# Kernel optimization log

Hardware: AMD Instinct MI355X
Metric: run time of the kernel (lower is better)

## Reference

```python
import jax, jax.numpy as jnp
import numpy as np

N, S, F, E, H, O, L, FE = 8, 1024, 64, 512, 8, 64, 6, 4
HD = E // H
FF = FE * E


def setup_inputs() -> dict:
    key = jax.random.key(0)
    ks = iter(jax.random.split(key, 40))
    def rn(shape, s=0.02):
        return jax.random.normal(next(ks), shape, jnp.float32) * s
    return {
        'x': jax.random.normal(next(ks), (N, F, S), jnp.float32),
        'W_first': rn((F, E)), 'b_first': jnp.zeros((E,), jnp.float32),
        'pos_emb': rn((S, E)),
        'Wq': rn((L, HD, HD)), 'bq': jnp.zeros((L, HD), jnp.float32),
        'Wk': rn((L, HD, HD)), 'bk': jnp.zeros((L, HD), jnp.float32),
        'Wv': rn((L, HD, HD)), 'bv': jnp.zeros((L, HD), jnp.float32),
        'Wo': rn((L, E, E)), 'bo': jnp.zeros((L, E), jnp.float32),
        'g1': jnp.ones((L, E), jnp.float32), 'be1': jnp.zeros((L, E), jnp.float32),
        'Wf1': rn((L, E, FF)), 'bf1': jnp.zeros((L, FF), jnp.float32),
        'Wf2': rn((L, FF, E)), 'bf2': jnp.zeros((L, E), jnp.float32),
        'g2': jnp.ones((L, E), jnp.float32), 'be2': jnp.zeros((L, E), jnp.float32),
        'Wfin': rn((E, O)), 'bfin': jnp.zeros((O,), jnp.float32),
    }


def layernorm(x, g, b, eps=1e-5):
    m = jnp.mean(x, axis=-1, keepdims=True)
    v = jnp.mean(jnp.square(x - m), axis=-1, keepdims=True)
    return (x - m) * jax.lax.rsqrt(v + eps) * g + b


def reference(x, W_first, b_first, pos_emb, Wq, bq, Wk, bk, Wv, bv, Wo, bo,
              g1, be1, Wf1, bf1, Wf2, bf2, g2, be2, Wfin, bfin):
    # x: (N, F, S) -> (N, S, F)
    h = jax.nn.relu(jnp.einsum('nfs,fe->nse', x, W_first) + b_first) + pos_emb[None]
    scale = E ** 0.5  # note: module scales by sqrt(embed_size), not sqrt(head_dim)
    for i in range(L):
        t = h.reshape(N, S, H, HD)
        q = jnp.einsum('nshd,de->nshe', t, Wq[i]) + bq[i]
        k = jnp.einsum('nshd,de->nshe', t, Wk[i]) + bk[i]
        v = jnp.einsum('nshd,de->nshe', t, Wv[i]) + bv[i]
        energy = jnp.einsum('nqhd,nkhd->nhqk', q, k)  # (N,H,S,S)
        att = jax.nn.softmax(energy / scale, axis=-1)
        o = jnp.einsum('nhqk,nkhd->nqhd', att, v).reshape(N, S, E)
        o = jnp.einsum('nse,ef->nsf', o, Wo[i]) + bo[i]
        hx = layernorm(o + h, g1[i], be1[i])
        ff = jax.nn.relu(jnp.einsum('nse,ef->nsf', hx, Wf1[i]) + bf1[i])
        ff = jnp.einsum('nsf,fe->nse', ff, Wf2[i]) + bf2[i]
        h = layernorm(ff + hx, g2[i], be2[i])
    # Conv1d kernel_size=1 == pointwise linear over channels; output (N, O, S)
    return jnp.einsum('nse,eo->nos', h, Wfin) + bfin[None, :, None]
```

## Files before the change

### kernel.cpp

```cpp
#include <hip/hip_runtime.h>
#include <hip/hip_bf16.h>
#include <math.h>

#define N_ 8
#define S_ 1024
#define F_ 64
#define E_ 512
#define H_ 8
#define O_ 64
#define L_ 6
#define HD_ 64
#define FF_ 2048
#define SCALE_ 0.044194173824159216f
#define LOG2E_ 1.4426950408889634f
#define QSCALE_ (SCALE_ * LOG2E_)

typedef unsigned short u16;
typedef __attribute__((ext_vector_type(8))) unsigned short u16x8;
typedef __attribute__((ext_vector_type(8))) short short8;
typedef __attribute__((ext_vector_type(4))) float floatx4;

__device__ __forceinline__ u16 f2b(float f) {
    union { float f; unsigned u; } v; v.f = f;
    unsigned u = v.u;
    unsigned r = (u + 0x7FFFu + ((u >> 16) & 1u)) >> 16;
    return (u16)r;
}
__device__ __forceinline__ u16 f2b_fast(float f) {
    union { float f; unsigned u; } v; v.f = f;
    return (u16)((v.u + 0x8000u) >> 16);
}
__device__ __forceinline__ int pperm(int row) {
    return ((2 * (row >> 2) + 5 * (row & 3)) & 7) | ((row & 2) << 2);
}

__global__ __launch_bounds__(256) void first_mfma(
    const float* __restrict__ x, const u16* __restrict__ wt,
    const float* __restrict__ bf, const float* __restrict__ pe,
    float* __restrict__ hout, u16* __restrict__ hb)
{
    __shared__ u16 a_s[128][72];
    int t = threadIdx.x;
    int w = t >> 6, lane = t & 63, quad = lane >> 4, c16 = lane & 15;
    int rowhalf = w >> 1, colhalf = w & 1;
    int col0 = blockIdx.x * 128;
    int row0 = blockIdx.y * 128;
    int n = row0 >> 10, s0 = row0 & 1023;

    const float* xb = x + (size_t)n * F_ * S_ + s0;
    #pragma unroll
    for (int i = 0; i < 8; i++) {
        int pos = (t + i * 256) * 4;
        int f = pos >> 7, sl = pos & 127;
        float4 v = *(const float4*)&xb[(size_t)f * S_ + sl];
        a_s[sl + 0][f] = f2b_fast(v.x);
        a_s[sl + 1][f] = f2b_fast(v.y);
        a_s[sl + 2][f] = f2b_fast(v.z);
        a_s[sl + 3][f] = f2b_fast(v.w);
    }
    __syncthreads();

    floatx4 acc[4][4];
    #pragma unroll
    for (int mt = 0; mt < 4; mt++)
        #pragma unroll
        for (int nt = 0; nt < 4; nt++) acc[mt][nt] = (floatx4){0.f, 0.f, 0.f, 0.f};

    #pragma unroll
    for (int ks = 0; ks < 2; ks++) {
        short8 af[4], bfr[4];
        #pragma unroll
        for (int mt = 0; mt < 4; mt++)
            af[mt] = *(const short8*)&a_s[rowhalf * 64 + mt * 16 + c16][ks * 32 + quad * 8];
        #pragma unroll
        for (int nt = 0; nt < 4; nt++)
            bfr[nt] = *(const short8*)&wt[(size_t)(col0 + colhalf * 64 + nt * 16 + c16) * F_
                                          + ks * 32 + quad * 8];
        #pragma unroll
        for (int mt = 0; mt < 4; mt++)
            #pragma unroll
            for (int nt = 0; nt < 4; nt++)
                acc[mt][nt] = __builtin_amdgcn_mfma_f32_16x16x32_bf16(
                    af[mt], bfr[nt], acc[mt][nt], 0, 0, 0);
    }

    #pragma unroll
    for (int nt = 0; nt < 4; nt++) {
        int col = col0 + colhalf * 64 + nt * 16 + c16;
        float bv = bf[col];
        #pragma unroll
        for (int mt = 0; mt < 4; mt++) {
            #pragma unroll
            for (int r = 0; r < 4; r++) {
                size_t row = (size_t)row0 + rowhalf * 64 + mt * 16 + quad * 4 + r;
                int s = (int)(row & 1023);
                float v = fmaxf(acc[mt][nt][r] + bv, 0.f) + pe[(size_t)s * E_ + col];
                hout[row * E_ + col] = v;
                hb[row * E_ + col] = f2b_fast(v);
            }
        }
    }
}

__global__ __launch_bounds__(256) void wcast_t(
    const float* __restrict__ W0, u16* __restrict__ Wt0, int K, int Nc)
{
    __shared__ float tile[32][33];
    int t = threadIdx.x;
    int bx = blockIdx.x, by = blockIdx.y;
    const float* W = W0 + (size_t)blockIdx.z * K * Nc;
    u16* Wt = Wt0 + (size_t)blockIdx.z * K * Nc;
    #pragma unroll
    for (int i = 0; i < 4; i++) {
        int q = t + i * 256; int r = q >> 5, c = q & 31;
        tile[r][c] = W[(size_t)(by * 32 + r) * Nc + bx * 32 + c];
    }
    __syncthreads();
    #pragma unroll
    for (int i = 0; i < 4; i++) {
        int q = t + i * 256; int r = q >> 5, c = q & 31;
        Wt[(size_t)(bx * 32 + r) * K + by * 32 + c] = f2b(tile[c][r]);
    }
}

__global__ __launch_bounds__(256) void qkvw_cast(
    const float* __restrict__ Wq, const float* __restrict__ Wk,
    const float* __restrict__ Wv,
    u16* __restrict__ wqt, u16* __restrict__ wkt, u16* __restrict__ wvt)
{
    int l = blockIdx.x;
    int t = threadIdx.x;
    size_t off = (size_t)l * HD_ * HD_;
    #pragma unroll
    for (int i = 0; i < 16; i++) {
        int idx = t + i * 256;
        int e = idx >> 6, d = idx & 63;
        wqt[off + idx] = f2b(Wq[off + d * HD_ + e]);
        wkt[off + idx] = f2b(Wk[off + d * HD_ + e]);
        wvt[off + idx] = f2b(Wv[off + d * HD_ + e]);
    }
}

__global__ __launch_bounds__(256) void qkv_mfma(
    const u16* __restrict__ hb,
    const u16* __restrict__ wqt, const u16* __restrict__ wkt,
    const u16* __restrict__ wvt,
    const float* __restrict__ bq, const float* __restrict__ bk,
    const float* __restrict__ bv,
    u16* __restrict__ qo, u16* __restrict__ ko, u16* __restrict__ vo)
{
    __shared__ u16 a_s[256][72];
    int t = threadIdx.x;
    int w = t >> 6, lane = t & 63, quad = lane >> 4, c16 = lane & 15;
    size_t row0 = (size_t)blockIdx.x * 256;

    #pragma unroll
    for (int i = 0; i < 8; i++) {
        int q = t + i * 256; int r = q >> 3, c = q & 7;
        *(u16x8*)&a_s[r][c * 8] = *(const u16x8*)&hb[(row0 + r) * HD_ + c * 8];
    }
    __syncthreads();

    short8 af[4][2];
    #pragma unroll
    for (int mt = 0; mt < 4; mt++)
        #pragma unroll
        for (int ks = 0; ks < 2; ks++)
            af[mt][ks] = *(const short8*)&a_s[w * 64 + mt * 16 + c16][ks * 32 + quad * 8];

    const u16* wts[3] = {wqt, wkt, wvt};
    const float* bs[3] = {bq, bk, bv};
    u16* outs[3] = {qo, ko, vo};

    #pragma unroll
    for (int m = 0; m < 3; m++) {
        short8 bfr[4][2];
        #pragma unroll
        for (int nt = 0; nt < 4; nt++)
            #pragma unroll
            for (int ks = 0; ks < 2; ks++)
                bfr[nt][ks] = *(const short8*)&wts[m][(nt * 16 + c16) * HD_ + ks * 32 + quad * 8];
        floatx4 acc[4][4];
        #pragma unroll
        for (int mt = 0; mt < 4; mt++)
            #pragma unroll
            for (int nt = 0; nt < 4; nt++) acc[mt][nt] = (floatx4){0.f, 0.f, 0.f, 0.f};
        #pragma unroll
        for (int ks = 0; ks < 2; ks++)
            #pragma unroll
            for (int mt = 0; mt < 4; mt++)
                #pragma unroll
                for (int nt = 0; nt < 4; nt++)
                    acc[mt][nt] = __builtin_amdgcn_mfma_f32_16x16x32_bf16(
                        af[mt][ks], bfr[nt][ks], acc[mt][nt], 0, 0, 0);
        float osc = (m == 0) ? QSCALE_ : 1.0f;
        #pragma unroll
        for (int nt = 0; nt < 4; nt++) {
            float bv_ = bs[m][nt * 16 + c16];
            #pragma unroll
            for (int mt = 0; mt < 4; mt++)
                #pragma unroll
                for (int r = 0; r < 4; r++)
                    outs[m][(row0 + w * 64 + mt * 16 + quad * 4 + r) * HD_ + nt * 16 + c16] =
                        f2b_fast((acc[mt][nt][r] + bv_) * osc);
        }
    }
}

__global__ __launch_bounds__(256) void vtrans(
    const u16* __restrict__ vb, u16* __restrict__ vt)
{
    int bid = blockIdx.x;
    int st = bid & 15, hh = (bid >> 4) & 7, n = bid >> 7;
    __shared__ u16 tile[64][72];
    int t = threadIdx.x;
    #pragma unroll
    for (int i = 0; i < 2; i++) {
        int q = t + i * 256; int sl = q >> 3, c = q & 7;
        *(u16x8*)&tile[sl][c * 8] =
            *(const u16x8*)&vb[(((size_t)(n * S_ + st * 64 + sl)) * H_ + hh) * 64 + c * 8];
    }
    __syncthreads();
    #pragma unroll
    for (int i = 0; i < 2; i++) {
        int q = t + i * 256; int d = q >> 3, sc = q & 7;
        u16x8 v;
        #pragma unroll
        for (int j = 0; j < 8; j++) v[j] = tile[sc * 8 + j][d];
        *(u16x8*)&vt[((size_t)(n * H_ + hh) * 64 + d) * (size_t)S_ + st * 64 + sc * 8] = v;
    }
}

__global__ __launch_bounds__(256, 2) void attn_mfma(
    const u16* __restrict__ Q, const u16* __restrict__ K,
    const u16* __restrict__ Vt, u16* __restrict__ O)
{
    int bid = blockIdx.x;
    int qt = bid & 7, hh = (bid >> 3) & 7, n = bid >> 6;
    int t = threadIdx.x;
    int w = t >> 6, lane = t & 63, quad = lane >> 4, c16 = lane & 15;

    __shared__ u16 qp_s[128][72];
    __shared__ u16 k_s[64][72];
    __shared__ u16 vt_s[64][72];
    u16 (*p_s)[72] = &qp_s[w * 32];

    const size_t qkbase = (size_t)n * S_ * E_ + hh * 64;
    const size_t vtbase = ((size_t)(n * H_ + hh) * 64) * (size_t)S_;

    #pragma unroll
    for (int i = 0; i < 4; i++) {
        int q = t + i * 256; int r = q >> 3, c = q & 7;
        *(u16x8*)&qp_s[r][c * 8] =
            *(const u16x8*)&Q[qkbase + (size_t)(qt * 128 + r) * E_ + c * 8];
    }
    __syncthreads();

    short8 af[2][2];
    #pragma unroll
    for (int mt = 0; mt < 2; mt++)
        #pragma unroll
        for (int ks = 0; ks < 2; ks++)
            af[mt][ks] = *(const short8*)&qp_s[w * 32 + mt * 16 + c16][ks * 32 + quad * 8];

    const short8 ones = {(short)0x3F80, (short)0x3F80, (short)0x3F80, (short)0x3F80,
                         (short)0x3F80, (short)0x3F80, (short)0x3F80, (short)0x3F80};
    const int pr = pperm(c16);
    int pw[4];
    #pragma unroll
    for (int r = 0; r < 4; r++) pw[r] = pperm(quad * 4 + r);

    floatx4 oacc[2][4], lacc[2];
    #pragma unroll
    for (int mt = 0; mt < 2; mt++) {
        lacc[mt] = (floatx4){0.f, 0.f, 0.f, 0.f};
        #pragma unroll
        for (int nt = 0; nt < 4; nt++) oacc[mt][nt] = (floatx4){0.f, 0.f, 0.f, 0.f};
    }

    int ar = t >> 3, acq = (t & 7) * 8;
    u16x8 pk[2], pv[2];
    #pragma unroll
    for (int i = 0; i < 2; i++) {
        pk[i] = *(const u16x8*)&K[qkbase + (size_t)(ar + i * 32) * E_ + acq];
        pv[i] = *(const u16x8*)&Vt[vtbase + (size_t)(ar + i * 32) * S_ + acq];
    }

    for (int k0 = 0; k0 < S_; k0 += 64) {
        #pragma unroll
        for (int i = 0; i < 2; i++) {
            *(u16x8*)&k_s[ar + i * 32][acq] = pk[i];
            *(u16x8*)&vt_s[ar + i * 32][acq] = pv[i];
        }
        __syncthreads();
        if (k0 + 64 < S_) {
            #pragma unroll
            for (int i = 0; i < 2; i++) {
                pk[i] = *(const u16x8*)&K[qkbase + (size_t)(k0 + 64 + ar + i * 32) * E_ + acq];
                pv[i] = *(const u16x8*)&Vt[vtbase + (size_t)(ar + i * 32) * S_ + k0 + 64 + acq];
            }
        }

        floatx4 sc[2][4];
        #pragma unroll
        for (int mt = 0; mt < 2; mt++)
            #pragma unroll
            for (int nt = 0; nt < 4; nt++) sc[mt][nt] = (floatx4){0.f, 0.f, 0.f, 0.f};
        #pragma unroll
        for (int ks = 0; ks < 2; ks++) {
            short8 bfr[4];
            #pragma unroll
            for (int nt = 0; nt < 4; nt++)
                bfr[nt] = *(const short8*)&k_s[nt * 16 + c16][ks * 32 + quad * 8];
            #pragma unroll
            for (int mt = 0; mt < 2; mt++)
                #pragma unroll
                for (int nt = 0; nt < 4; nt++)
                    sc[mt][nt] = __builtin_amdgcn_mfma_f32_16x16x32_bf16(
                        af[mt][ks], bfr[nt], sc[mt][nt], 0, 0, 0);
        }

        #pragma unroll
        for (int mt = 0; mt < 2; mt++)
            #pragma unroll
            for (int nt = 0; nt < 4; nt++)
                #pragma unroll
                for (int r = 0; r < 4; r++)
                    p_s[mt * 16 + pw[r]][nt * 16 + c16] =
                        f2b_fast(exp2f(sc[mt][nt][r]));

        #pragma unroll
        for (int ks = 0; ks < 2; ks++) {
            short8 vf[4];
            #pragma unroll
            for (int nt = 0; nt < 4; nt++)
                vf[nt] = *(const short8*)&vt_s[nt * 16 + c16][ks * 32 + quad * 8];
            #pragma unroll
            for (int mt = 0; mt < 2; mt++) {
                short8 pf = *(const short8*)&p_s[mt * 16 + pr][ks * 32 + quad * 8];
                lacc[mt] = __builtin_amdgcn_mfma_f32_16x16x32_bf16(pf, ones, lacc[mt], 0, 0, 0);
                #pragma unroll
                for (int nt = 0; nt < 4; nt++)
                    oacc[mt][nt] = __builtin_amdgcn_mfma_f32_16x16x32_bf16(
                        pf, vf[nt], oacc[mt][nt], 0, 0, 0);
            }
        }
        __syncthreads();
    }

    #pragma unroll
    for (int mt = 0; mt < 2; mt++)
        #pragma unroll
        for (int r = 0; r < 4; r++) {
            float rl = 1.f / lacc[mt][r];
            int s = qt * 128 + w * 32 + mt * 16 + quad * 4 + r;
            size_t base = (size_t)(n * S_ + s) * E_ + hh * 64;
            #pragma unroll
            for (int nt = 0; nt < 4; nt++)
                O[base + nt * 16 + c16] = f2b_fast(oacc[mt][nt][r] * rl);
        }
}

template <int MT, bool RELU, bool HASRES, bool OUTF32, bool OUTBF16>
__global__ __launch_bounds__(256, 2) void gemm_mfma(
    const u16* __restrict__ A, const u16* __restrict__ Bt,
    const float* __restrict__ bias, const float* __restrict__ resid,
    float* __restrict__ outf, u16* __restrict__ outb, int M, int Nc, int K)
{
    constexpr int MTILES = MT / 32;
    __shared__ u16 a_s[MT][72];
    __shared__ u16 b_s[128][72];
    int t = threadIdx.x;
    int w = t >> 6, lane = t & 63, quad = lane >> 4, c16 = lane & 15;
    int rowhalf = w >> 1, colhalf = w & 1;
    size_t row0 = (size_t)blockIdx.y * MT;
    size_t col0 = (size_t)blockIdx.x * 128;

    floatx4 acc[MTILES][4];
    #pragma unroll
    for (int mt = 0; mt < MTILES; mt++)
        #pragma unroll
        for (int nt = 0; nt < 4; nt++) acc[mt][nt] = (floatx4){0.f, 0.f, 0.f, 0.f};

    int ar = t >> 3, acq = (t & 7) * 8;
    u16x8 pa[MTILES], pb[4];
    #pragma unroll
    for (int i = 0; i < MTILES; i++)
        pa[i] = *(const u16x8*)&A[(row0 + ar + i * 32) * K + acq];
    #pragma unroll
    for (int i = 0; i < 4; i++)
        pb[i] = *(const u16x8*)&Bt[(col0 + ar + i * 32) * K + acq];

    for (int k0 = 0; k0 < K; k0 += 64) {
        #pragma unroll
        for (int i = 0; i < MTILES; i++)
            *(u16x8*)&a_s[ar + i * 32][acq] = pa[i];
        #pragma unroll
        for (int i = 0; i < 4; i++)
            *(u16x8*)&b_s[ar + i * 32][acq] = pb[i];
        __syncthreads();
        if (k0 + 64 < K) {
            #pragma unroll
            for (int i = 0; i < MTILES; i++)
                pa[i] = *(const u16x8*)&A[(row0 + ar + i * 32) * K + k0 + 64 + acq];
            #pragma unroll
            for (int i = 0; i < 4; i++)
                pb[i] = *(const u16x8*)&Bt[(col0 + ar + i * 32) * K + k0 + 64 + acq];
        }
        #pragma unroll
        for (int ks = 0; ks < 2; ks++) {
            short8 af[MTILES], bf[4];
            #pragma unroll
            for (int mt = 0; mt < MTILES; mt++)
                af[mt] = *(const short8*)&a_s[rowhalf * (MT / 2) + mt * 16 + c16][ks * 32 + quad * 8];
            #pragma unroll
            for (int nt = 0; nt < 4; nt++)
                bf[nt] = *(const short8*)&b_s[colhalf * 64 + nt * 16 + c16][ks * 32 + quad * 8];
            #pragma unroll
            for (int mt = 0; mt < MTILES; mt++)
                #pragma unroll
                for (int nt = 0; nt < 4; nt++)
                    acc[mt][nt] = __builtin_amdgcn_mfma_f32_16x16x32_bf16(
                        af[mt], bf[nt], acc[mt][nt], 0, 0, 0);
        }
        __syncthreads();
    }

    #pragma unroll
    for (int nt = 0; nt < 4; nt++) {
        int col = (int)col0 + colhalf * 64 + nt * 16 + c16;
        float bv = bias[col];
        #pragma unroll
        for (int mt = 0; mt < MTILES; mt++) {
            size_t rowb = row0 + rowhalf * (MT / 2) + mt * 16 + quad * 4;
            #pragma unroll
            for (int r = 0; r < 4; r++) {
                size_t row = rowb + r;
                float v = acc[mt][nt][r] + bv;
                if constexpr (HASRES) v += resid[row * Nc + col];
                if constexpr (RELU) v = fmaxf(v, 0.f);
                if constexpr (OUTF32) outf[row * Nc + col] = v;
                if constexpr (OUTBF16) outb[row * Nc + col] = f2b_fast(v);
            }
        }
    }
}

template <bool EMITB>
__global__ __launch_bounds__(256) void layernorm_k(
    const float* __restrict__ in, const float* __restrict__ g,
    const float* __restrict__ bb, float* __restrict__ out, u16* __restrict__ outb)
{
    int row = blockIdx.x;
    int t = threadIdx.x;
    const float* x = in + (size_t)row * E_;
    float x0 = x[t], x1 = x[t + 256];
    float s = x0 + x1;
    #pragma unroll
    for (int off = 32; off; off >>= 1) s += __shfl_down(s, off, 64);
    __shared__ float red[4];
    int wid = t >> 6, lane = t & 63;
    if (lane == 0) red[wid] = s;
    __syncthreads();
    float m = (red[0] + red[1] + red[2] + red[3]) * (1.f / E_);
    float d0 = x0 - m, d1 = x1 - m;
    float sq = d0 * d0 + d1 * d1;
    #pragma unroll
    for (int off = 32; off; off >>= 1) sq += __shfl_down(sq, off, 64);
    __syncthreads();
    if (lane == 0) red[wid] = sq;
    __syncthreads();
    float var = (red[0] + red[1] + red[2] + red[3]) * (1.f / E_);
    float rstd = rsqrtf(var + 1e-5f);
    float o0 = d0 * rstd * g[t] + bb[t];
    float o1 = d1 * rstd * g[t + 256] + bb[t + 256];
    out[(size_t)row * E_ + t] = o0;
    out[(size_t)row * E_ + t + 256] = o1;
    if constexpr (EMITB) {
        outb[(size_t)row * E_ + t] = f2b_fast(o0);
        outb[(size_t)row * E_ + t + 256] = f2b_fast(o1);
    }
}

__global__ __launch_bounds__(256) void final_mfma(
    const u16* __restrict__ hb, const u16* __restrict__ wft,
    const float* __restrict__ bfin, float* __restrict__ outp)
{
    __shared__ u16 a_s[64][72];
    int t = threadIdx.x;
    int w = t >> 6, lane = t & 63, quad = lane >> 4, c16 = lane & 15;
    size_t row0 = (size_t)blockIdx.x * 64;

    floatx4 acc[4];
    #pragma unroll
    for (int nt = 0; nt < 4; nt++) acc[nt] = (floatx4){0.f, 0.f, 0.f, 0.f};

    int ar = t >> 3, acq = (t & 7) * 8;
    u16x8 pa[2];
    #pragma unroll
    for (int i = 0; i < 2; i++)
        pa[i] = *(const u16x8*)&hb[(row0 + ar + i * 32) * E_ + acq];

    for (int k0 = 0; k0 < E_; k0 += 64) {
        #pragma unroll
        for (int i = 0; i < 2; i++)
            *(u16x8*)&a_s[ar + i * 32][acq] = pa[i];
        __syncthreads();
        if (k0 + 64 < E_) {
            #pragma unroll
            for (int i = 0; i < 2; i++)
                pa[i] = *(const u16x8*)&hb[(row0 + ar + i * 32) * E_ + k0 + 64 + acq];
        }
        #pragma unroll
        for (int ks = 0; ks < 2; ks++) {
            short8 af = *(const short8*)&a_s[w * 16 + c16][ks * 32 + quad * 8];
            #pragma unroll
            for (int nt = 0; nt < 4; nt++) {
                short8 bf = *(const short8*)&wft[(nt * 16 + c16) * E_ + k0 + ks * 32 + quad * 8];
                acc[nt] = __builtin_amdgcn_mfma_f32_16x16x32_bf16(af, bf, acc[nt], 0, 0, 0);
            }
        }
        __syncthreads();
    }

    #pragma unroll
    for (int nt = 0; nt < 4; nt++) {
        int o = nt * 16 + c16;
        float bv = bfin[o];
        #pragma unroll
        for (int r = 0; r < 4; r++) {
            size_t row = row0 + w * 16 + quad * 4 + r;
            int n = (int)(row >> 10), s = (int)(row & 1023);
            outp[((size_t)(n * O_ + o)) * S_ + s] = acc[nt][r] + bv;
        }
    }
}

extern "C" void kernel_launch(void* const* d_in, const int* in_sizes, int n_in,
                              void* d_out, int out_size, void* d_ws, size_t ws_size,
                              hipStream_t stream)
{
    const float* x       = (const float*)d_in[0];
    const float* W_first = (const float*)d_in[1];
    const float* b_first = (const float*)d_in[2];
    const float* pos_emb = (const float*)d_in[3];
    const float* Wq      = (const float*)d_in[4];
    const float* bq      = (const float*)d_in[5];
    const float* Wk      = (const float*)d_in[6];
    const float* bk      = (const float*)d_in[7];
    const float* Wv      = (const float*)d_in[8];
    const float* bv      = (const float*)d_in[9];
    const float* Wo      = (const float*)d_in[10];
    const float* bo      = (const float*)d_in[11];
    const float* g1      = (const float*)d_in[12];
    const float* be1     = (const float*)d_in[13];
    const float* Wf1     = (const float*)d_in[14];
    const float* bf1     = (const float*)d_in[15];
    const float* Wf2     = (const float*)d_in[16];
    const float* bf2     = (const float*)d_in[17];
    const float* g2      = (const float*)d_in[18];
    const float* be2     = (const float*)d_in[19];
    const float* Wfin    = (const float*)d_in[20];
    const float* bfin    = (const float*)d_in[21];
    float* out = (float*)d_out;

    const size_t M4 = (size_t)N_ * S_ * E_;
    float* hbuf = (float*)d_ws;
    float* t1   = hbuf + M4;
    float* hx   = t1 + M4;
    u16*   hxb  = (u16*)(hx + M4);
    u16*   hb   = hxb;
    u16*   qb   = hxb + M4;
    u16*   kb   = qb + M4;
    u16*   vb   = kb + M4;
    u16*   vt   = vb + M4;
    u16*   ob   = vt + M4;
    u16*   ffb  = qb;
    u16*   wot  = ob + M4;
    u16*   wf1t = wot + (size_t)L_ * E_ * E_;
    u16*   wf2t = wf1t + (size_t)L_ * E_ * FF_;
    u16*   wqt  = wf2t + (size_t)L_ * FF_ * E_;
    u16*   wkt  = wqt + (size_t)L_ * HD_ * HD_;
    u16*   wvt  = wkt + (size_t)L_ * HD_ * HD_;
    u16*   wft  = wvt + (size_t)L_ * HD_ * HD_;
    u16*   w1t  = wft + (size_t)O_ * E_;

    const int rows = N_ * S_;

    qkvw_cast<<<L_, 256, 0, stream>>>(Wq, Wk, Wv, wqt, wkt, wvt);
    wcast_t<<<dim3(E_ / 32, F_ / 32, 1), 256, 0, stream>>>(W_first, w1t, F_, E_);
    wcast_t<<<dim3(E_ / 32, E_ / 32, L_), 256, 0, stream>>>(Wo, wot, E_, E_);
    wcast_t<<<dim3(FF_ / 32, E_ / 32, L_), 256, 0, stream>>>(Wf1, wf1t, E_, FF_);
    wcast_t<<<dim3(E_ / 32, FF_ / 32, L_), 256, 0, stream>>>(Wf2, wf2t, FF_, E_);
    wcast_t<<<dim3(O_ / 32, E_ / 32, 1), 256, 0, stream>>>(Wfin, wft, E_, O_);

    first_mfma<<<dim3(E_ / 128, rows / 128), 256, 0, stream>>>(
        x, w1t, b_first, pos_emb, hbuf, hb);

    for (int i = 0; i < L_; i++) {
        qkv_mfma<<<256, 256, 0, stream>>>(
            hb, wqt + (size_t)i * HD_ * HD_, wkt + (size_t)i * HD_ * HD_,
            wvt + (size_t)i * HD_ * HD_, bq + i * HD_, bk + i * HD_, bv + i * HD_,
            qb, kb, vb);
        vtrans<<<1024, 256, 0, stream>>>(vb, vt);
        attn_mfma<<<512, 256, 0, stream>>>(qb, kb, vt, ob);
        gemm_mfma<64, false, true, true, false><<<dim3(E_ / 128, rows / 64), 256, 0, stream>>>(
            ob, wot + (size_t)i * E_ * E_, bo + i * E_, hbuf, t1, nullptr, rows, E_, E_);
        layernorm_k<true><<<rows, 256, 0, stream>>>(t1, g1 + i * E_, be1 + i * E_, hx, hxb);
        gemm_mfma<128, true, false, false, true><<<dim3(FF_ / 128, rows / 128), 256, 0, stream>>>(
            hxb, wf1t + (size_t)i * E_ * FF_, bf1 + i * FF_, nullptr, nullptr, ffb,
            rows, FF_, E_);
        gemm_mfma<64, false, true, true, false><<<dim3(E_ / 128, rows / 64), 256, 0, stream>>>(
            ffb, wf2t + (size_t)i * FF_ * E_, bf2 + i * E_, hx, t1, nullptr,
            rows, E_, FF_);
        layernorm_k<true><<<rows, 256, 0, stream>>>(t1, g2 + i * E_, be2 + i * E_, hbuf, hb);
    }

    final_mfma<<<rows / 64, 256, 0, stream>>>(hb, wft, bfin, out);
}
```

Before: 1.044 ms.

## Keep residual stream in bf16 only and halve attention query tile

The fp32 residual copies are dropped. The residual stream now lives only in a single bf16 buffer, and the GEMM epilogues read it through a bf16-to-float conversion. This cuts the fp32 writes from layernorm and first_mfma and halves the residual reads. Separately, the attention kernel now uses 64-query tiles with one 16-row m-tile per wave, launching 1024 blocks instead of 512 for more parallelism, at the cost of reloading K/V tiles twice as often. Holding the residual in bf16 lowers accuracy across the six layers.

```diff
diff --git a/kernel.cpp b/kernel.cpp
--- a/kernel.cpp
+++ b/kernel.cpp
@@ -30,6 +30,10 @@
     union { float f; unsigned u; } v; v.f = f;
     return (u16)((v.u + 0x8000u) >> 16);
 }
+__device__ __forceinline__ float b2f(u16 h) {
+    union { unsigned u; float f; } v; v.u = ((unsigned)h) << 16;
+    return v.f;
+}
 __device__ __forceinline__ int pperm(int row) {
     return ((2 * (row >> 2) + 5 * (row & 3)) & 7) | ((row & 2) << 2);
 }
@@ -37,7 +41,7 @@
 __global__ __launch_bounds__(256) void first_mfma(
     const float* __restrict__ x, const u16* __restrict__ wt,
     const float* __restrict__ bf, const float* __restrict__ pe,
-    float* __restrict__ hout, u16* __restrict__ hb)
+    u16* __restrict__ resb)
 {
     __shared__ u16 a_s[128][72];
     int t = threadIdx.x;
@@ -95,8 +99,7 @@
                 size_t row = (size_t)row0 + rowhalf * 64 + mt * 16 + quad * 4 + r;
                 int s = (int)(row & 1023);
                 float v = fmaxf(acc[mt][nt][r] + bv, 0.f) + pe[(size_t)s * E_ + col];
-                hout[row * E_ + col] = v;
-                hb[row * E_ + col] = f2b_fast(v);
+                resb[row * E_ + col] = f2b_fast(v);
             }
         }
     }
@@ -236,32 +239,30 @@
     const u16* __restrict__ Vt, u16* __restrict__ O)
 {
     int bid = blockIdx.x;
-    int qt = bid & 7, hh = (bid >> 3) & 7, n = bid >> 6;
+    int qt = bid & 15, hh = (bid >> 4) & 7, n = bid >> 7;
     int t = threadIdx.x;
     int w = t >> 6, lane = t & 63, quad = lane >> 4, c16 = lane & 15;
 
-    __shared__ u16 qp_s[128][72];
+    __shared__ u16 qp_s[64][72];
     __shared__ u16 k_s[64][72];
     __shared__ u16 vt_s[64][72];
-    u16 (*p_s)[72] = &qp_s[w * 32];
+    u16 (*p_s)[72] = &qp_s[w * 16];
 
     const size_t qkbase = (size_t)n * S_ * E_ + hh * 64;
     const size_t vtbase = ((size_t)(n * H_ + hh) * 64) * (size_t)S_;
 
     #pragma unroll
-    for (int i = 0; i < 4; i++) {
+    for (int i = 0; i < 2; i++) {
         int q = t + i * 256; int r = q >> 3, c = q & 7;
         *(u16x8*)&qp_s[r][c * 8] =
-            *(const u16x8*)&Q[qkbase + (size_t)(qt * 128 + r) * E_ + c * 8];
-    }
-    __syncthreads();
-
-    short8 af[2][2];
-    #pragma unroll
-    for (int mt = 0; mt < 2; mt++)
-        #pragma unroll
-        for (int ks = 0; ks < 2; ks++)
-            af[mt][ks] = *(const short8*)&qp_s[w * 32 + mt * 16 + c16][ks * 32 + quad * 8];
+            *(const u16x8*)&Q[qkbase + (size_t)(qt * 64 + r) * E_ + c * 8];
+    }
+    __syncthreads();
+
+    short8 af[2];
+    #pragma unroll
+    for (int ks = 0; ks < 2; ks++)
+        af[ks] = *(const short8*)&qp_s[w * 16 + c16][ks * 32 + quad * 8];
 
     const short8 ones = {(short)0x3F80, (short)0x3F80, (short)0x3F80, (short)0x3F80,
                          (short)0x3F80, (short)0x3F80, (short)0x3F80, (short)0x3F80};
@@ -270,13 +271,10 @@
     #pragma unroll
     for (int r = 0; r < 4; r++) pw[r] = pperm(quad * 4 + r);
 
-    floatx4 oacc[2][4], lacc[2];
-    #pragma unroll
-    for (int mt = 0; mt < 2; mt++) {
-        lacc[mt] = (floatx4){0.f, 0.f, 0.f, 0.f};
-        #pragma unroll
-        for (int nt = 0; nt < 4; nt++) oacc[mt][nt] = (floatx4){0.f, 0.f, 0.f, 0.f};
-    }
+    floatx4 oacc[4], lacc;
+    lacc = (floatx4){0.f, 0.f, 0.f, 0.f};
+    #pragma unroll
+    for (int nt = 0; nt < 4; nt++) oacc[nt] = (floatx4){0.f, 0.f, 0.f, 0.f};
 
     int ar = t >> 3, acq = (t & 7) * 8;
     u16x8 pk[2], pv[2];
@@ -301,11 +299,9 @@
             }
         }
 
-        floatx4 sc[2][4];
-        #pragma unroll
-        for (int mt = 0; mt < 2; mt++)
-            #pragma unroll
-            for (int nt = 0; nt < 4; nt++) sc[mt][nt] = (floatx4){0.f, 0.f, 0.f, 0.f};
+        floatx4 sc[4];
+        #pragma unroll
+        for (int nt = 0; nt < 4; nt++) sc[nt] = (floatx4){0.f, 0.f, 0.f, 0.f};
         #pragma unroll
         for (int ks = 0; ks < 2; ks++) {
             short8 bfr[4];
@@ -313,21 +309,15 @@
             for (int nt = 0; nt < 4; nt++)
                 bfr[nt] = *(const short8*)&k_s[nt * 16 + c16][ks * 32 + quad * 8];
             #pragma unroll
-            for (int mt = 0; mt < 2; mt++)
-                #pragma unroll
-                for (int nt = 0; nt < 4; nt++)
-                    sc[mt][nt] = __builtin_amdgcn_mfma_f32_16x16x32_bf16(
-                        af[mt][ks], bfr[nt], sc[mt][nt], 0, 0, 0);
-        }
-
-        #pragma unroll
-        for (int mt = 0; mt < 2; mt++)
-            #pragma unroll
             for (int nt = 0; nt < 4; nt++)
-                #pragma unroll
-                for (int r = 0; r < 4; r++)
-                    p_s[mt * 16 + pw[r]][nt * 16 + c16] =
-                        f2b_fast(exp2f(sc[mt][nt][r]));
+                sc[nt] = __builtin_amdgcn_mfma_f32_16x16x32_bf16(af[ks], bfr[nt], sc[nt], 0, 0, 0);
+        }
+
+        #pragma unroll
+        for (int nt = 0; nt < 4; nt++)
+            #pragma unroll
+            for (int r = 0; r < 4; r++)
+                p_s[pw[r]][nt * 16 + c16] = f2b_fast(exp2f(sc[nt][r]));
 
         #pragma unroll
         for (int ks = 0; ks < 2; ks++) {
@@ -335,36 +325,30 @@
             #pragma unroll
             for (int nt = 0; nt < 4; nt++)
                 vf[nt] = *(const short8*)&vt_s[nt * 16 + c16][ks * 32 + quad * 8];
-            #pragma unroll
-            for (int mt = 0; mt < 2; mt++) {
-                short8 pf = *(const short8*)&p_s[mt * 16 + pr][ks * 32 + quad * 8];
-                lacc[mt] = __builtin_amdgcn_mfma_f32_16x16x32_bf16(pf, ones, lacc[mt], 0, 0, 0);
-                #pragma unroll
-                for (int nt = 0; nt < 4; nt++)
-                    oacc[mt][nt] = __builtin_amdgcn_mfma_f32_16x16x32_bf16(
-                        pf, vf[nt], oacc[mt][nt], 0, 0, 0);
-            }
+            short8 pf = *(const short8*)&p_s[pr][ks * 32 + quad * 8];
+            lacc = __builtin_amdgcn_mfma_f32_16x16x32_bf16(pf, ones, lacc, 0, 0, 0);
+            #pragma unroll
+            for (int nt = 0; nt < 4; nt++)
+                oacc[nt] = __builtin_amdgcn_mfma_f32_16x16x32_bf16(pf, vf[nt], oacc[nt], 0, 0, 0);
         }
         __syncthreads();
     }
 
     #pragma unroll
-    for (int mt = 0; mt < 2; mt++)
-        #pragma unroll
-        for (int r = 0; r < 4; r++) {
-            float rl = 1.f / lacc[mt][r];
-            int s = qt * 128 + w * 32 + mt * 16 + quad * 4 + r;
-            size_t base = (size_t)(n * S_ + s) * E_ + hh * 64;
-            #pragma unroll
-            for (int nt = 0; nt < 4; nt++)
-                O[base + nt * 16 + c16] = f2b_fast(oacc[mt][nt][r] * rl);
-        }
+    for (int r = 0; r < 4; r++) {
+        float rl = 1.f / lacc[r];
+        int s = qt * 64 + w * 16 + quad * 4 + r;
+        size_t base = (size_t)(n * S_ + s) * E_ + hh * 64;
+        #pragma unroll
+        for (int nt = 0; nt < 4; nt++)
+            O[base + nt * 16 + c16] = f2b_fast(oacc[nt][r] * rl);
+    }
 }
 
 template <int MT, bool RELU, bool HASRES, bool OUTF32, bool OUTBF16>
 __global__ __launch_bounds__(256, 2) void gemm_mfma(
     const u16* __restrict__ A, const u16* __restrict__ Bt,
-    const float* __restrict__ bias, const float* __restrict__ resid,
+    const float* __restrict__ bias, const u16* __restrict__ resid,
     float* __restrict__ outf, u16* __restrict__ outb, int M, int Nc, int K)
 {
     constexpr int MTILES = MT / 32;
@@ -437,7 +421,7 @@
             for (int r = 0; r < 4; r++) {
                 size_t row = rowb + r;
                 float v = acc[mt][nt][r] + bv;
-                if constexpr (HASRES) v += resid[row * Nc + col];
+                if constexpr (HASRES) v += b2f(resid[row * Nc + col]);
                 if constexpr (RELU) v = fmaxf(v, 0.f);
                 if constexpr (OUTF32) outf[row * Nc + col] = v;
                 if constexpr (OUTBF16) outb[row * Nc + col] = f2b_fast(v);
@@ -446,10 +430,9 @@
     }
 }
 
-template <bool EMITB>
 __global__ __launch_bounds__(256) void layernorm_k(
     const float* __restrict__ in, const float* __restrict__ g,
-    const float* __restrict__ bb, float* __restrict__ out, u16* __restrict__ outb)
+    const float* __restrict__ bb, u16* __restrict__ outb)
 {
     int row = blockIdx.x;
     int t = threadIdx.x;
@@ -472,14 +455,8 @@
     __syncthreads();
     float var = (red[0] + red[1] + red[2] + red[3]) * (1.f / E_);
     float rstd = rsqrtf(var + 1e-5f);
-    float o0 = d0 * rstd * g[t] + bb[t];
-    float o1 = d1 * rstd * g[t + 256] + bb[t + 256];
-    out[(size_t)row * E_ + t] = o0;
-    out[(size_t)row * E_ + t + 256] = o1;
-    if constexpr (EMITB) {
-        outb[(size_t)row * E_ + t] = f2b_fast(o0);
-        outb[(size_t)row * E_ + t + 256] = f2b_fast(o1);
-    }
+    outb[(size_t)row * E_ + t] = f2b_fast(d0 * rstd * g[t] + bb[t]);
+    outb[(size_t)row * E_ + t + 256] = f2b_fast(d1 * rstd * g[t + 256] + bb[t + 256]);
 }
 
 __global__ __launch_bounds__(256) void final_mfma(
@@ -565,12 +542,9 @@
     float* out = (float*)d_out;
 
     const size_t M4 = (size_t)N_ * S_ * E_;
-    float* hbuf = (float*)d_ws;
-    float* t1   = hbuf + M4;
-    float* hx   = t1 + M4;
-    u16*   hxb  = (u16*)(hx + M4);
-    u16*   hb   = hxb;
-    u16*   qb   = hxb + M4;
+    float* t1   = (float*)d_ws;
+    u16*   resb = (u16*)(t1 + M4);
+    u16*   qb   = resb + M4;
     u16*   kb   = qb + M4;
     u16*   vb   = kb + M4;
     u16*   vt   = vb + M4;
@@ -595,26 +569,26 @@
     wcast_t<<<dim3(O_ / 32, E_ / 32, 1), 256, 0, stream>>>(Wfin, wft, E_, O_);
 
     first_mfma<<<dim3(E_ / 128, rows / 128), 256, 0, stream>>>(
-        x, w1t, b_first, pos_emb, hbuf, hb);
+        x, w1t, b_first, pos_emb, resb);
 
     for (int i = 0; i < L_; i++) {
         qkv_mfma<<<256, 256, 0, stream>>>(
-            hb, wqt + (size_t)i * HD_ * HD_, wkt + (size_t)i * HD_ * HD_,
+            resb, wqt + (size_t)i * HD_ * HD_, wkt + (size_t)i * HD_ * HD_,
             wvt + (size_t)i * HD_ * HD_, bq + i * HD_, bk + i * HD_, bv + i * HD_,
             qb, kb, vb);
         vtrans<<<1024, 256, 0, stream>>>(vb, vt);
-        attn_mfma<<<512, 256, 0, stream>>>(qb, kb, vt, ob);
+        attn_mfma<<<1024, 256, 0, stream>>>(qb, kb, vt, ob);
         gemm_mfma<64, false, true, true, false><<<dim3(E_ / 128, rows / 64), 256, 0, stream>>>(
-            ob, wot + (size_t)i * E_ * E_, bo + i * E_, hbuf, t1, nullptr, rows, E_, E_);
-        layernorm_k<true><<<rows, 256, 0, stream>>>(t1, g1 + i * E_, be1 + i * E_, hx, hxb);
+            ob, wot + (size_t)i * E_ * E_, bo + i * E_, resb, t1, nullptr, rows, E_, E_);
+        layernorm_k<<<rows, 256, 0, stream>>>(t1, g1 + i * E_, be1 + i * E_, resb);
         gemm_mfma<128, true, false, false, true><<<dim3(FF_ / 128, rows / 128), 256, 0, stream>>>(
-            hxb, wf1t + (size_t)i * E_ * FF_, bf1 + i * FF_, nullptr, nullptr, ffb,
+            resb, wf1t + (size_t)i * E_ * FF_, bf1 + i * FF_, nullptr, nullptr, ffb,
             rows, FF_, E_);
         gemm_mfma<64, false, true, true, false><<<dim3(E_ / 128, rows / 64), 256, 0, stream>>>(
-            ffb, wf2t + (size_t)i * FF_ * E_, bf2 + i * E_, hx, t1, nullptr,
+            ffb, wf2t + (size_t)i * FF_ * E_, bf2 + i * E_, resb, t1, nullptr,
             rows, E_, FF_);
-        layernorm_k<true><<<rows, 256, 0, stream>>>(t1, g2 + i * E_, be2 + i * E_, hbuf, hb);
-    }
-
-    final_mfma<<<rows / 64, 256, 0, stream>>>(hb, wft, bfin, out);
-}
+        layernorm_k<<<rows, 256, 0, stream>>>(t1, g2 + i * E_, be2 + i * E_, resb);
+    }
+
+    final_mfma<<<rows / 64, 256, 0, stream>>>(resb, wft, bfin, out);
+}
```

Result: no change. 1.044 ms (-0.0%).
